# Optimization experiments

Hardware: AMD Instinct MI355X
Metric: run time of the kernel (lower is better)

The kernel has to match this reference:

```python
import jax, jax.numpy as jnp
import numpy as np

K = 512      # per-token feature dim (also per-head dim in this module)
H = 8        # heads
B = 2
T = 2048


def setup_inputs() -> dict:
    key = jax.random.key(0)
    ks = jax.random.split(key, 6)
    s = 1.0 / np.sqrt(K)
    x = jax.random.normal(ks[0], (B, T, K), dtype=jnp.float32)
    # torch Linear(k, k*heads, bias=False): y = x @ W with W stored here as [in, out]
    Wq = jax.random.uniform(ks[1], (K, K * H), dtype=jnp.float32, minval=-s, maxval=s)
    Wk = jax.random.uniform(ks[2], (K, K * H), dtype=jnp.float32, minval=-s, maxval=s)
    Wv = jax.random.uniform(ks[3], (K, K * H), dtype=jnp.float32, minval=-s, maxval=s)
    su = 1.0 / np.sqrt(K * H)
    Wu = jax.random.uniform(ks[4], (K * H, K), dtype=jnp.float32, minval=-su, maxval=su)
    bu = jax.random.uniform(ks[5], (K,), dtype=jnp.float32, minval=-su, maxval=su)
    return {"x": x, "Wq": Wq, "Wk": Wk, "Wv": Wv, "Wu": Wu, "bu": bu}


def reference(x, Wq, Wk, Wv, Wu, bu):
    b, t, k = x.shape
    h = H
    # project and split heads: [b, t, h, k] -> [b, h, t, k]
    q = (x @ Wq).reshape(b, t, h, k).transpose(0, 2, 1, 3)
    kk = (x @ Wk).reshape(b, t, h, k).transpose(0, 2, 1, 3)
    v = (x @ Wv).reshape(b, t, h, k).transpose(0, 2, 1, 3)
    scale = k ** (-0.25)  # applied to both q and k, matching source
    dot = jnp.einsum('bhqd,bhkd->bhqk', q * scale, kk * scale)
    attn = jax.nn.softmax(dot, axis=-1)
    out = jnp.einsum('bhqk,bhkd->bhqd', attn, v)          # [b, h, t, k]
    out = out.transpose(0, 2, 1, 3).reshape(b, t, h * k)   # [b, t, h*k]
    return out @ Wu + bu
```

## Files before the change

kernel.cpp:

```cpp
#include <hip/hip_runtime.h>

typedef unsigned short u16;
typedef unsigned short ushort8 __attribute__((ext_vector_type(8)));
typedef unsigned short us4 __attribute__((ext_vector_type(4)));
typedef __bf16 bf16x8 __attribute__((ext_vector_type(8)));
typedef float f32x4 __attribute__((ext_vector_type(4)));

#define DEV static __device__ __forceinline__

DEV u16 f2bf(float f) {
    unsigned int u = __builtin_bit_cast(unsigned int, f);
    u += 0x7FFFu + ((u >> 16) & 1u);
    return (u16)(u >> 16);
}

DEV f32x4 mfma16(ushort8 a, ushort8 b, f32x4 c) {
    return __builtin_amdgcn_mfma_f32_16x16x32_bf16((bf16x8)a, (bf16x8)b, c, 0, 0, 0);
}

DEV void gload_lds16(const void* g, void* l) {
    __builtin_amdgcn_global_load_lds(
        (const __attribute__((address_space(1))) void*)g,
        (__attribute__((address_space(3))) void*)l, 16, 0, 0);
}

__global__ void cvt_kernel(const float* __restrict__ in, u16* __restrict__ out, int n) {
    int i = (blockIdx.x * 256 + threadIdx.x) * 4;
    if (i >= n) return;
    float4 f = *(const float4*)(in + i);
    us4 o;
    o.x = f2bf(f.x); o.y = f2bf(f.y); o.z = f2bf(f.z); o.w = f2bf(f.w);
    *(us4*)(out + i) = o;
}

__global__ void transpose_cvt(const float* __restrict__ in, u16* __restrict__ out, int R, int C) {
    __shared__ u16 tile[64][72];
    int c0 = blockIdx.x << 6, r0 = blockIdx.y << 6;
    int tx = threadIdx.x & 63, ty = threadIdx.x >> 6;
    for (int i = 0; i < 64; i += 4) {
        int r = i + ty;
        tile[r][tx] = f2bf(in[(size_t)(r0 + r) * C + c0 + tx]);
    }
    __syncthreads();
    for (int i = 0; i < 64; i += 4) {
        int r = i + ty;
        out[(size_t)(c0 + r) * R + r0 + tx] = tile[tx][r];
    }
}

__global__ void transpose_bh(const u16* __restrict__ in, u16* __restrict__ out) {
    __shared__ u16 tile[64][72];
    int bh = blockIdx.z;
    int d0 = blockIdx.x << 6, t0 = blockIdx.y << 6;
    int tx = threadIdx.x & 63, ty = threadIdx.x >> 6;
    const u16* src = in + (size_t)bh * 2048 * 512;
    u16* dst = out + (size_t)bh * 512 * 2048;
    for (int i = 0; i < 64; i += 4) {
        int r = i + ty;
        tile[r][tx] = src[(size_t)(t0 + r) * 512 + d0 + tx];
    }
    __syncthreads();
    for (int i = 0; i < 64; i += 4) {
        int r = i + ty;
        dst[(size_t)(d0 + r) * 2048 + t0 + tx] = tile[tx][r];
    }
}

template <int MODE>
__launch_bounds__(256, 2)
__global__ void gemm_bt(const u16* __restrict__ A, const u16* __restrict__ Bt,
                        float scale, const float* __restrict__ bias,
                        void* __restrict__ out, int Kc) {
    __shared__ u16 Asub[128 * 32];
    __shared__ u16 Bsub[128 * 32];
    const int tid = threadIdx.x, lane = tid & 63, wv = tid >> 6;
    const int bm = blockIdx.y << 7, bn = blockIdx.x << 7;
    const int wr = (wv >> 1) << 6, wc = (wv & 1) << 6;
    const int lr = lane & 15, hi = lane >> 4;

    f32x4 acc[4][4] = {};

    int off0 = (wv * 2048 + lane * 16) >> 1;
    int row0 = off0 >> 5, k0e = off0 & 31;
    int off1 = off0 + 512;
    int row1 = off1 >> 5, k1e = off1 & 31;

    const u16* Ag0 = A + (size_t)(bm + row0) * Kc + k0e;
    const u16* Ag1 = A + (size_t)(bm + row1) * Kc + k1e;
    const u16* Bg0 = Bt + (size_t)(bn + row0) * Kc + k0e;
    const u16* Bg1 = Bt + (size_t)(bn + row1) * Kc + k1e;

    for (int kk = 0; kk < Kc; kk += 32) {
        __syncthreads();
        gload_lds16(Ag0 + kk, &Asub[wv * 1024]);
        gload_lds16(Ag1 + kk, &Asub[wv * 1024 + 512]);
        gload_lds16(Bg0 + kk, &Bsub[wv * 1024]);
        gload_lds16(Bg1 + kk, &Bsub[wv * 1024 + 512]);
        __syncthreads();

        ushort8 a[4], b[4];
#pragma unroll
        for (int m = 0; m < 4; ++m)
            a[m] = *(const ushort8*)&Asub[(wr + m * 16 + lr) * 32 + hi * 8];
#pragma unroll
        for (int n = 0; n < 4; ++n)
            b[n] = *(const ushort8*)&Bsub[(wc + n * 16 + lr) * 32 + hi * 8];
#pragma unroll
        for (int m = 0; m < 4; ++m)
#pragma unroll
            for (int n = 0; n < 4; ++n)
                acc[m][n] = mfma16(a[m], b[n], acc[m][n]);
    }

#pragma unroll
    for (int m = 0; m < 4; ++m)
#pragma unroll
        for (int n = 0; n < 4; ++n)
#pragma unroll
            for (int r = 0; r < 4; ++r) {
                int row = bm + wr + m * 16 + hi * 4 + r;
                int col = bn + wc + n * 16 + lr;
                float v = acc[m][n][r] * scale;
                if constexpr (MODE == 0) {
                    size_t dst = ((size_t)((row >> 11) * 8 + (col >> 9)) * 2048 + (row & 2047)) * 512
                                 + (col & 511);
                    ((u16*)out)[dst] = f2bf(v);
                } else {
                    ((float*)out)[(size_t)row * 512 + col] = v + bias[col];
                }
            }
}

__launch_bounds__(512, 2)
__global__ void attn_kernel(const u16* __restrict__ Q, const u16* __restrict__ K,
                            const u16* __restrict__ Vt, u16* __restrict__ O) {
    __shared__ u16 Klds[2][32 * 512];
    __shared__ u16 Plds[2][128 * 40];
    __shared__ __align__(16) float red[2][128];
    __shared__ __align__(16) float lred[128];
    __shared__ int rflag[2][8];

    const int tid = threadIdx.x, lane = tid & 63, wv = tid >> 6;
    const int lr = lane & 15, hi = lane >> 4;
    const int qh = wv >> 2, ds = wv & 3;

    const int flat = blockIdx.x;
    const int nid = (flat & 7) * 32 + (flat >> 3);
    const int bh = nid >> 4;
    const int q0 = (nid & 15) << 7;

    ushort8 qf[16];
    {
        const char* Qg = (const char*)(Q + ((size_t)bh * 2048 + q0 + wv * 16 + lr) * 512) + hi * 16;
#pragma unroll
        for (int ks = 0; ks < 16; ++ks) qf[ks] = *(const ushort8*)(Qg + ks * 64);
    }

    f32x4 acc[4][8] = {};
    float mrun = -1e30f, lrun = 0.f;

    const char* Kg = (const char*)(K + (size_t)bh * 2048 * 512);
    const char* Vg = (const char*)(Vt + (size_t)bh * 512 * 2048);

#pragma unroll
    for (int r4 = 0; r4 < 4; ++r4) {
        int r = wv * 4 + r4;
        gload_lds16(Kg + (size_t)r * 1024 + ((lane ^ (r & 7)) << 4),
                    &Klds[0][(size_t)r * 512]);
    }
    __syncthreads();

    for (int t = 0; t < 64; ++t) {
        const int kt = t << 5;
        const int cb = t & 1;

        if (t + 1 < 64) {
            const char* Kgt = Kg + (size_t)(kt + 32) * 1024;
#pragma unroll
            for (int r4 = 0; r4 < 4; ++r4) {
                int r = wv * 4 + r4;
                gload_lds16(Kgt + (size_t)r * 1024 + ((lane ^ (r & 7)) << 4),
                            &Klds[cb ^ 1][(size_t)r * 512]);
            }
        }

        f32x4 s0a = {}, s0b = {}, s1a = {}, s1b = {};
        const char* Kb = (const char*)&Klds[cb][0];
        __builtin_amdgcn_s_setprio(1);
#pragma unroll
        for (int ks = 0; ks < 8; ++ks) {
            int swz0 = (ks * 64 + hi * 16) ^ ((lr & 7) << 4);
            int swz1 = ((ks + 8) * 64 + hi * 16) ^ ((lr & 7) << 4);
            ushort8 kf0a = *(const ushort8*)(Kb + lr * 1024 + swz0);
            ushort8 kf1a = *(const ushort8*)(Kb + (lr + 16) * 1024 + swz0);
            ushort8 kf0b = *(const ushort8*)(Kb + lr * 1024 + swz1);
            ushort8 kf1b = *(const ushort8*)(Kb + (lr + 16) * 1024 + swz1);
            s0a = mfma16(kf0a, qf[ks], s0a);
            s1a = mfma16(kf1a, qf[ks], s1a);
            s0b = mfma16(kf0b, qf[ks + 8], s0b);
            s1b = mfma16(kf1b, qf[ks + 8], s1b);
        }
        __builtin_amdgcn_s_setprio(0);
        f32x4 s0, s1;
#pragma unroll
        for (int r = 0; r < 4; ++r) { s0[r] = s0a[r] + s0b[r]; s1[r] = s1a[r] + s1b[r]; }

        float mx = fmaxf(fmaxf(fmaxf(s0[0], s0[1]), fmaxf(s0[2], s0[3])),
                         fmaxf(fmaxf(s1[0], s1[1]), fmaxf(s1[2], s1[3])));
        mx = fmaxf(mx, __shfl_xor(mx, 16));
        mx = fmaxf(mx, __shfl_xor(mx, 32));
        float a = 1.0f;
        bool upd = false;
        if (mx > mrun + 11.5f) { a = exp2f(mrun - mx); mrun = mx; upd = true; }
        float p[8];
#pragma unroll
        for (int r = 0; r < 4; ++r) {
            p[r]     = exp2f(s0[r] - mrun);
            p[4 + r] = exp2f(s1[r] - mrun);
        }
        float ps = ((p[0] + p[1]) + (p[2] + p[3])) + ((p[4] + p[5]) + (p[6] + p[7]));
        ps += __shfl_xor(ps, 16);
        ps += __shfl_xor(ps, 32);
        lrun = lrun * a + ps;

        {
            const int qr = wv * 16 + lr;
            char* Pb = (char*)&Plds[cb][0] + qr * 80;
            uint2 w01, w23;
            w01.x = (unsigned)f2bf(p[0]) | ((unsigned)f2bf(p[1]) << 16);
            w01.y = (unsigned)f2bf(p[2]) | ((unsigned)f2bf(p[3]) << 16);
            w23.x = (unsigned)f2bf(p[4]) | ((unsigned)f2bf(p[5]) << 16);
            w23.y = (unsigned)f2bf(p[6]) | ((unsigned)f2bf(p[7]) << 16);
            *(uint2*)(Pb + hi * 8) = w01;
            *(uint2*)(Pb + 32 + hi * 8) = w23;
            if (hi == 0) red[cb][qr] = a;
        }
        if (lane == 0) rflag[cb][wv] = __any(upd) ? 1 : 0;

        __syncthreads();

        int anyupd = rflag[cb][0] | rflag[cb][1] | rflag[cb][2] | rflag[cb][3]
                   | rflag[cb][4] | rflag[cb][5] | rflag[cb][6] | rflag[cb][7];
        if (anyupd) {
#pragma unroll
            for (int mf = 0; mf < 4; ++mf) {
                f32x4 a4 = *(const f32x4*)&red[cb][qh * 64 + mf * 16 + hi * 4];
#pragma unroll
                for (int nf = 0; nf < 8; ++nf)
#pragma unroll
                    for (int r = 0; r < 4; ++r) acc[mf][nf][r] *= a4[r];
            }
        }

        ushort8 pf[4];
#pragma unroll
        for (int mf = 0; mf < 4; ++mf)
            pf[mf] = *(const ushort8*)((const char*)&Plds[cb][0]
                                       + (qh * 64 + mf * 16 + lr) * 80 + hi * 16);
        __builtin_amdgcn_s_setprio(1);
#pragma unroll
        for (int nf = 0; nf < 8; ++nf) {
            int d = ds * 128 + nf * 16 + lr;
            ushort8 vf = *(const ushort8*)(Vg + (size_t)d * 4096 + (size_t)kt * 2 + hi * 16);
#pragma unroll
            for (int mf = 0; mf < 4; ++mf) acc[mf][nf] = mfma16(pf[mf], vf, acc[mf][nf]);
        }
        __builtin_amdgcn_s_setprio(0);
    }

    if (hi == 0) lred[wv * 16 + lr] = lrun;
    __syncthreads();

    const int b = bh >> 3, h = bh & 7;
#pragma unroll
    for (int mf = 0; mf < 4; ++mf) {
        f32x4 lv = *(const f32x4*)&lred[qh * 64 + mf * 16 + hi * 4];
        f32x4 inv;
#pragma unroll
        for (int r = 0; r < 4; ++r) inv[r] = 1.0f / lv[r];
#pragma unroll
        for (int nf = 0; nf < 8; ++nf) {
            int d = ds * 128 + nf * 16 + lr;
#pragma unroll
            for (int r = 0; r < 4; ++r) {
                int t = q0 + qh * 64 + mf * 16 + hi * 4 + r;
                O[((size_t)(b * 2048 + t)) * 4096 + h * 512 + d] = f2bf(acc[mf][nf][r] * inv[r]);
            }
        }
    }
}

extern "C" void kernel_launch(void* const* d_in, const int* in_sizes, int n_in,
                              void* d_out, int out_size, void* d_ws, size_t ws_size,
                              hipStream_t stream) {
    const float* x  = (const float*)d_in[0];
    const float* Wq = (const float*)d_in[1];
    const float* Wk = (const float*)d_in[2];
    const float* Wv = (const float*)d_in[3];
    const float* Wu = (const float*)d_in[4];
    const float* bu = (const float*)d_in[5];

    char* ws = (char*)d_ws;
    const size_t MB = 1ull << 20;
    u16* xb  = (u16*)(ws + 0);
    u16* Wqt = (u16*)(ws + 4 * MB);
    u16* Wkt = (u16*)(ws + 8 * MB);
    u16* Wvt = (u16*)(ws + 12 * MB);
    u16* Wut = (u16*)(ws + 16 * MB);
    u16* Qb  = (u16*)(ws + 20 * MB);
    u16* Kb  = (u16*)(ws + 52 * MB);
    u16* Vb  = (u16*)(ws + 84 * MB);
    u16* Vtb = (u16*)(ws + 116 * MB);
    u16* Ob  = (u16*)(ws + 84 * MB);

    cvt_kernel<<<2048, 256, 0, stream>>>(x, xb, 2 * 2048 * 512);
    transpose_cvt<<<dim3(64, 8), 256, 0, stream>>>(Wq, Wqt, 512, 4096);
    transpose_cvt<<<dim3(64, 8), 256, 0, stream>>>(Wk, Wkt, 512, 4096);
    transpose_cvt<<<dim3(64, 8), 256, 0, stream>>>(Wv, Wvt, 512, 4096);
    transpose_cvt<<<dim3(8, 64), 256, 0, stream>>>(Wu, Wut, 4096, 512);

    const float s2 = 0.06375871593f;
    gemm_bt<0><<<dim3(32, 32), 256, 0, stream>>>(xb, Wqt, s2,   nullptr, Qb, 512);
    gemm_bt<0><<<dim3(32, 32), 256, 0, stream>>>(xb, Wkt, 1.0f, nullptr, Kb, 512);
    gemm_bt<0><<<dim3(32, 32), 256, 0, stream>>>(xb, Wvt, 1.0f, nullptr, Vb, 512);

    transpose_bh<<<dim3(8, 32, 16), 256, 0, stream>>>(Vb, Vtb);

    attn_kernel<<<256, 512, 0, stream>>>(Qb, Kb, Vtb, Ob);

    gemm_bt<1><<<dim3(4, 32), 256, 0, stream>>>(Ob, Wut, 1.0f, bu, d_out, 4096);
}
```

Before: 541.0 us.

## Triple-buffer K tiles with two-ahead prefetch and hoist V loads early

Extends the K LDS ring from two to three buffers and prefetches K tiles two iterations ahead. The block-wide __syncthreads is replaced by explicit vmcnt/lgkmcnt waits plus s_barrier, so newer loads can stay in flight across the barrier. V fragments for the iteration are loaded at its start, before the QK^T MFMAs, so the global latency overlaps with compute. The cost is more LDS (an extra 32 KB buffer, which may affect two blocks per CU) and more VGPRs for vf[8], and correctness now depends on hand-counted vmcnt values.

```diff
diff --git a/kernel.cpp b/kernel.cpp
--- a/kernel.cpp
+++ b/kernel.cpp
@@ -134,7 +134,7 @@
 __launch_bounds__(512, 2)
 __global__ void attn_kernel(const u16* __restrict__ Q, const u16* __restrict__ K,
                             const u16* __restrict__ Vt, u16* __restrict__ O) {
-    __shared__ u16 Klds[2][32 * 512];
+    __shared__ u16 Klds[3][32 * 512];
     __shared__ u16 Plds[2][128 * 40];
     __shared__ __align__(16) float red[2][128];
     __shared__ __align__(16) float lred[128];
@@ -163,29 +163,44 @@
     const char* Vg = (const char*)(Vt + (size_t)bh * 512 * 2048);
 
 #pragma unroll
-    for (int r4 = 0; r4 < 4; ++r4) {
-        int r = wv * 4 + r4;
-        gload_lds16(Kg + (size_t)r * 1024 + ((lane ^ (r & 7)) << 4),
-                    &Klds[0][(size_t)r * 512]);
-    }
-    __syncthreads();
-
+    for (int tt = 0; tt < 2; ++tt) {
+        const char* Kgt = Kg + (size_t)tt * 32 * 1024;
+#pragma unroll
+        for (int r4 = 0; r4 < 4; ++r4) {
+            int r = wv * 4 + r4;
+            gload_lds16(Kgt + (size_t)r * 1024 + ((lane ^ (r & 7)) << 4),
+                        &Klds[tt][(size_t)r * 512]);
+        }
+    }
+    asm volatile("s_waitcnt vmcnt(4)" ::: "memory");
+    __builtin_amdgcn_sched_barrier(0);
+    __builtin_amdgcn_s_barrier();
+
+    int kb = 0;
     for (int t = 0; t < 64; ++t) {
         const int kt = t << 5;
         const int cb = t & 1;
 
-        if (t + 1 < 64) {
-            const char* Kgt = Kg + (size_t)(kt + 32) * 1024;
+        ushort8 vf[8];
+#pragma unroll
+        for (int nf = 0; nf < 8; ++nf) {
+            int d = ds * 128 + nf * 16 + lr;
+            vf[nf] = *(const ushort8*)(Vg + (size_t)d * 4096 + (size_t)kt * 2 + hi * 16);
+        }
+
+        if (t + 2 < 64) {
+            const int kb2 = (kb >= 1) ? kb - 1 : 2;
+            const char* Kgt = Kg + (size_t)(kt + 64) * 1024;
 #pragma unroll
             for (int r4 = 0; r4 < 4; ++r4) {
                 int r = wv * 4 + r4;
                 gload_lds16(Kgt + (size_t)r * 1024 + ((lane ^ (r & 7)) << 4),
-                            &Klds[cb ^ 1][(size_t)r * 512]);
+                            &Klds[kb2][(size_t)r * 512]);
             }
         }
 
         f32x4 s0a = {}, s0b = {}, s1a = {}, s1b = {};
-        const char* Kb = (const char*)&Klds[cb][0];
+        const char* Kb = (const char*)&Klds[kb][0];
         __builtin_amdgcn_s_setprio(1);
 #pragma unroll
         for (int ks = 0; ks < 8; ++ks) {
@@ -237,7 +252,12 @@
         }
         if (lane == 0) rflag[cb][wv] = __any(upd) ? 1 : 0;
 
-        __syncthreads();
+        asm volatile("s_waitcnt lgkmcnt(0)" ::: "memory");
+        if (t < 62) { asm volatile("s_waitcnt vmcnt(12)" ::: "memory"); }
+        else        { asm volatile("s_waitcnt vmcnt(8)"  ::: "memory"); }
+        __builtin_amdgcn_sched_barrier(0);
+        __builtin_amdgcn_s_barrier();
+        __builtin_amdgcn_sched_barrier(0);
 
         int anyupd = rflag[cb][0] | rflag[cb][1] | rflag[cb][2] | rflag[cb][3]
                    | rflag[cb][4] | rflag[cb][5] | rflag[cb][6] | rflag[cb][7];
@@ -259,13 +279,12 @@
                                        + (qh * 64 + mf * 16 + lr) * 80 + hi * 16);
         __builtin_amdgcn_s_setprio(1);
 #pragma unroll
-        for (int nf = 0; nf < 8; ++nf) {
-            int d = ds * 128 + nf * 16 + lr;
-            ushort8 vf = *(const ushort8*)(Vg + (size_t)d * 4096 + (size_t)kt * 2 + hi * 16);
-#pragma unroll
-            for (int mf = 0; mf < 4; ++mf) acc[mf][nf] = mfma16(pf[mf], vf, acc[mf][nf]);
-        }
+        for (int nf = 0; nf < 8; ++nf)
+#pragma unroll
+            for (int mf = 0; mf < 4; ++mf) acc[mf][nf] = mfma16(pf[mf], vf[nf], acc[mf][nf]);
         __builtin_amdgcn_s_setprio(0);
+
+        kb = (kb == 2) ? 0 : kb + 1;
     }
 
     if (hi == 0) lred[wv * 16 + lr] = lrun;
```

New measurement: 580.7 us. +7.4%, slower.

## Software-pipeline QK^T of next tile with softmax and PV of previous

Applied to the files above, without the earlier changes.

Restructures the attention loop so the score MFMAs for key tile t are issued before the softmax and P·V work for tile t-1, all within one barrier interval. The goal is to hide the exp, reduction and LDS-store latency of softmax behind independent matrix-core work. The loop body is split into lambdas with a prologue and epilogue, and the score accumulation drops from four to two MFMA chains. That shortens the independent MFMA dependency chains and adds register pressure from carrying the previous tile's scores.

```diff
diff --git a/kernel.cpp b/kernel.cpp
--- a/kernel.cpp
+++ b/kernel.cpp
@@ -162,49 +162,20 @@
     const char* Kg = (const char*)(K + (size_t)bh * 2048 * 512);
     const char* Vg = (const char*)(Vt + (size_t)bh * 512 * 2048);
 
-#pragma unroll
-    for (int r4 = 0; r4 < 4; ++r4) {
-        int r = wv * 4 + r4;
-        gload_lds16(Kg + (size_t)r * 1024 + ((lane ^ (r & 7)) << 4),
-                    &Klds[0][(size_t)r * 512]);
-    }
-    __syncthreads();
-
-    for (int t = 0; t < 64; ++t) {
-        const int kt = t << 5;
-        const int cb = t & 1;
-
-        if (t + 1 < 64) {
-            const char* Kgt = Kg + (size_t)(kt + 32) * 1024;
-#pragma unroll
-            for (int r4 = 0; r4 < 4; ++r4) {
-                int r = wv * 4 + r4;
-                gload_lds16(Kgt + (size_t)r * 1024 + ((lane ^ (r & 7)) << 4),
-                            &Klds[cb ^ 1][(size_t)r * 512]);
-            }
-        }
-
-        f32x4 s0a = {}, s0b = {}, s1a = {}, s1b = {};
-        const char* Kb = (const char*)&Klds[cb][0];
-        __builtin_amdgcn_s_setprio(1);
-#pragma unroll
-        for (int ks = 0; ks < 8; ++ks) {
-            int swz0 = (ks * 64 + hi * 16) ^ ((lr & 7) << 4);
-            int swz1 = ((ks + 8) * 64 + hi * 16) ^ ((lr & 7) << 4);
-            ushort8 kf0a = *(const ushort8*)(Kb + lr * 1024 + swz0);
-            ushort8 kf1a = *(const ushort8*)(Kb + (lr + 16) * 1024 + swz0);
-            ushort8 kf0b = *(const ushort8*)(Kb + lr * 1024 + swz1);
-            ushort8 kf1b = *(const ushort8*)(Kb + (lr + 16) * 1024 + swz1);
-            s0a = mfma16(kf0a, qf[ks], s0a);
-            s1a = mfma16(kf1a, qf[ks], s1a);
-            s0b = mfma16(kf0b, qf[ks + 8], s0b);
-            s1b = mfma16(kf1b, qf[ks + 8], s1b);
-        }
-        __builtin_amdgcn_s_setprio(0);
-        f32x4 s0, s1;
-#pragma unroll
-        for (int r = 0; r < 4; ++r) { s0[r] = s0a[r] + s0b[r]; s1[r] = s1a[r] + s1b[r]; }
-
+    auto s_phase = [&](const char* Kb, f32x4& s0, f32x4& s1) {
+        s0 = (f32x4){0.f, 0.f, 0.f, 0.f};
+        s1 = (f32x4){0.f, 0.f, 0.f, 0.f};
+#pragma unroll
+        for (int ks = 0; ks < 16; ++ks) {
+            int swz = (ks * 64 + hi * 16) ^ ((lr & 7) << 4);
+            ushort8 kf0 = *(const ushort8*)(Kb + lr * 1024 + swz);
+            ushort8 kf1 = *(const ushort8*)(Kb + (lr + 16) * 1024 + swz);
+            s0 = mfma16(kf0, qf[ks], s0);
+            s1 = mfma16(kf1, qf[ks], s1);
+        }
+    };
+
+    auto softmax_store = [&](const f32x4& s0, const f32x4& s1, int pcb) {
         float mx = fmaxf(fmaxf(fmaxf(s0[0], s0[1]), fmaxf(s0[2], s0[3])),
                          fmaxf(fmaxf(s1[0], s1[1]), fmaxf(s1[2], s1[3])));
         mx = fmaxf(mx, __shfl_xor(mx, 16));
@@ -223,50 +194,82 @@
         ps += __shfl_xor(ps, 32);
         lrun = lrun * a + ps;
 
-        {
-            const int qr = wv * 16 + lr;
-            char* Pb = (char*)&Plds[cb][0] + qr * 80;
-            uint2 w01, w23;
-            w01.x = (unsigned)f2bf(p[0]) | ((unsigned)f2bf(p[1]) << 16);
-            w01.y = (unsigned)f2bf(p[2]) | ((unsigned)f2bf(p[3]) << 16);
-            w23.x = (unsigned)f2bf(p[4]) | ((unsigned)f2bf(p[5]) << 16);
-            w23.y = (unsigned)f2bf(p[6]) | ((unsigned)f2bf(p[7]) << 16);
-            *(uint2*)(Pb + hi * 8) = w01;
-            *(uint2*)(Pb + 32 + hi * 8) = w23;
-            if (hi == 0) red[cb][qr] = a;
-        }
-        if (lane == 0) rflag[cb][wv] = __any(upd) ? 1 : 0;
-
-        __syncthreads();
-
-        int anyupd = rflag[cb][0] | rflag[cb][1] | rflag[cb][2] | rflag[cb][3]
-                   | rflag[cb][4] | rflag[cb][5] | rflag[cb][6] | rflag[cb][7];
+        const int qr = wv * 16 + lr;
+        char* Pb = (char*)&Plds[pcb][0] + qr * 80;
+        uint2 w01, w23;
+        w01.x = (unsigned)f2bf(p[0]) | ((unsigned)f2bf(p[1]) << 16);
+        w01.y = (unsigned)f2bf(p[2]) | ((unsigned)f2bf(p[3]) << 16);
+        w23.x = (unsigned)f2bf(p[4]) | ((unsigned)f2bf(p[5]) << 16);
+        w23.y = (unsigned)f2bf(p[6]) | ((unsigned)f2bf(p[7]) << 16);
+        *(uint2*)(Pb + hi * 8) = w01;
+        *(uint2*)(Pb + 32 + hi * 8) = w23;
+        if (hi == 0) red[pcb][qr] = a;
+        if (lane == 0) rflag[pcb][wv] = __any(upd) ? 1 : 0;
+    };
+
+    auto pv_phase = [&](int pcb, int ktv) {
+        int anyupd = rflag[pcb][0] | rflag[pcb][1] | rflag[pcb][2] | rflag[pcb][3]
+                   | rflag[pcb][4] | rflag[pcb][5] | rflag[pcb][6] | rflag[pcb][7];
         if (anyupd) {
 #pragma unroll
             for (int mf = 0; mf < 4; ++mf) {
-                f32x4 a4 = *(const f32x4*)&red[cb][qh * 64 + mf * 16 + hi * 4];
+                f32x4 a4 = *(const f32x4*)&red[pcb][qh * 64 + mf * 16 + hi * 4];
 #pragma unroll
                 for (int nf = 0; nf < 8; ++nf)
 #pragma unroll
                     for (int r = 0; r < 4; ++r) acc[mf][nf][r] *= a4[r];
             }
         }
-
         ushort8 pf[4];
 #pragma unroll
         for (int mf = 0; mf < 4; ++mf)
-            pf[mf] = *(const ushort8*)((const char*)&Plds[cb][0]
+            pf[mf] = *(const ushort8*)((const char*)&Plds[pcb][0]
                                        + (qh * 64 + mf * 16 + lr) * 80 + hi * 16);
         __builtin_amdgcn_s_setprio(1);
 #pragma unroll
         for (int nf = 0; nf < 8; ++nf) {
             int d = ds * 128 + nf * 16 + lr;
-            ushort8 vf = *(const ushort8*)(Vg + (size_t)d * 4096 + (size_t)kt * 2 + hi * 16);
+            ushort8 vf = *(const ushort8*)(Vg + (size_t)d * 4096 + (size_t)ktv * 2 + hi * 16);
 #pragma unroll
             for (int mf = 0; mf < 4; ++mf) acc[mf][nf] = mfma16(pf[mf], vf, acc[mf][nf]);
         }
         __builtin_amdgcn_s_setprio(0);
-    }
+    };
+
+    auto prefetch_k = [&](int tt) {
+        const char* Kgt = Kg + (size_t)tt * 32 * 1024;
+#pragma unroll
+        for (int r4 = 0; r4 < 4; ++r4) {
+            int r = wv * 4 + r4;
+            gload_lds16(Kgt + (size_t)r * 1024 + ((lane ^ (r & 7)) << 4),
+                        &Klds[tt & 1][(size_t)r * 512]);
+        }
+    };
+
+    f32x4 s0c, s1c, s0p, s1p;
+
+    prefetch_k(0);
+    __syncthreads();
+
+    prefetch_k(1);
+    s_phase((const char*)&Klds[0][0], s0c, s1c);
+    __syncthreads();
+
+    for (int t = 1; t < 64; ++t) {
+        if (t + 1 < 64) prefetch_k(t + 1);
+
+        s0p = s0c; s1p = s1c;
+        s_phase((const char*)&Klds[t & 1][0], s0c, s1c);
+        softmax_store(s0p, s1p, (t - 1) & 1);
+
+        __syncthreads();
+
+        pv_phase((t - 1) & 1, (t - 1) << 5);
+    }
+
+    softmax_store(s0c, s1c, 1);
+    __syncthreads();
+    pv_phase(1, 63 << 5);
 
     if (hi == 0) lred[wv * 16 + lr] = lrun;
     __syncthreads();
```

After: 497.8 us. 8.0% less time.
